# Kernel optimization log

Measured on AMD Instinct MI355X. Metric: run time of the kernel, lower is better.

## Reference

```python
import jax, jax.numpy as jnp
import numpy as np

B, C, V = 65536, 2, 3          # batch of coords, coord_dim, value_dim
D, K, S = 64, 1024, 4          # latent_dim, num_codes, num_latent_vectors (VQ stages)
H, L, F = 1024, 5, 25          # hidden_size, num_layers, num_freqs
IN = C * (2 * F + 1)           # 102: positional-encoded decoder input
COMMIT = 0.25


def setup_inputs() -> dict:
    key = jax.random.key(0)
    ks = jax.random.split(key, 12)
    coords = jax.random.uniform(ks[0], (B, C), jnp.float32, -1.0, 1.0)
    latents = jax.random.normal(ks[1], (1, S, D), jnp.float32)
    cb = jax.random.normal(ks[2], (S, K, D), jnp.float32)
    codebooks = cb / jnp.linalg.norm(cb, axis=-1, keepdims=True)  # unit-norm init as in module
    mod_W = jax.random.normal(ks[3], (L, D, H), jnp.float32) / np.sqrt(D)
    mod_b = jax.random.normal(ks[4], (L, H), jnp.float32) * 0.01
    dec_W0 = jax.random.normal(ks[5], (IN, H), jnp.float32) / np.sqrt(IN)
    dec_b0 = jax.random.normal(ks[6], (H,), jnp.float32) * 0.01
    dec_Wh = jax.random.normal(ks[7], (L - 1, H, H), jnp.float32) / np.sqrt(H)
    dec_bh = jax.random.normal(ks[8], (L - 1, H), jnp.float32) * 0.01
    dec_Wout = jax.random.normal(ks[9], (H, V), jnp.float32) / np.sqrt(H)
    dec_bout = jax.random.normal(ks[10], (V,), jnp.float32) * 0.01
    return dict(coords=coords, latent_idx=0, latents=latents, codebooks=codebooks,
                mod_W=mod_W, mod_b=mod_b, dec_W0=dec_W0, dec_b0=dec_b0,
                dec_Wh=dec_Wh, dec_bh=dec_bh, dec_Wout=dec_Wout, dec_bout=dec_bout)


def _vq(z, emb):
    # z: (1, D), emb: (K, D) -> squared-distance argmin + straight-through
    d = jnp.sum(z * z, axis=1, keepdims=True) - 2.0 * (z @ emb.T) + jnp.sum(emb * emb, axis=1)
    idx = jnp.argmin(d, axis=1)               # (1,)
    z_q = emb[idx]                            # (1, D)
    z_q_st = z_q + jax.lax.stop_gradient(z - z_q)   # fwd value == z, grad flows to embedding
    loss = COMMIT * jnp.mean((jax.lax.stop_gradient(z_q) - z) ** 2)
    return z_q_st, idx, loss


def reference(coords, latent_idx, latents, codebooks, mod_W, mod_b,
              dec_W0, dec_b0, dec_Wh, dec_bh, dec_Wout, dec_bout):
    img = latents[latent_idx]                 # (S, D)
    z_q_sum = jnp.zeros((1, D), coords.dtype)
    residual_target = jnp.zeros((1, D), coords.dtype)
    total_vq_loss = 0.0
    idxs = []
    for s in range(S):                        # residual VQ over fixed small #stages
        z_stage = img[s:s + 1]
        if s == 0:
            residual_target = z_stage
            z_cur = z_stage
        else:
            residual_target = residual_target + z_stage
            z_cur = residual_target - jax.lax.stop_gradient(z_q_sum)
        z_q_st, idx, l = _vq(z_cur, codebooks[s])
        z_q_sum = z_q_sum + z_q_st
        total_vq_loss = total_vq_loss + l
        idxs.append(idx)
    # modulation betas from the (same-for-all-rows) quantized latent; broadcast over B
    betas = jnp.einsum('od,ldh->loh', z_q_sum, mod_W) + mod_b[:, None, :]   # (L, 1, H)
    # positional encoding: [x, sin(pi*f0*x), cos(pi*f0*x), sin(pi*f1*x), ...]
    freqs = 2.0 ** jnp.arange(F, dtype=coords.dtype)
    ang = coords[:, None, :] * (freqs[None, :, None] * jnp.pi)              # (B, F, C)
    pe = jnp.concatenate(
        [coords, jnp.stack([jnp.sin(ang), jnp.cos(ang)], axis=2).reshape(coords.shape[0], -1)],
        axis=-1)                                                            # (B, IN)
    h = jax.nn.relu(pe @ dec_W0 + dec_b0 + betas[0])
    for i in range(L - 1):
        h = jax.nn.relu(h @ dec_Wh[i] + dec_bh[i] + betas[i + 1])
    values = h @ dec_Wout + dec_bout                                        # (B, V)
    return values, jnp.stack(idxs), total_vq_loss
```

## Files before the change

kernel.cpp:

```cpp
#include <hip/hip_runtime.h>
#include <hip/hip_bf16.h>
#include <stdint.h>

#define NB   65536
#define NC   2
#define NV   3
#define ND   64
#define NK   1024
#define NS   4
#define NH   1024
#define NL   5
#define NF   25
#define NIN  102
#define K0P  128

typedef float f32x4  __attribute__((ext_vector_type(4)));
typedef float f32x16 __attribute__((ext_vector_type(16)));
typedef int   i32x4  __attribute__((ext_vector_type(4)));
typedef int   i32x8  __attribute__((ext_vector_type(8)));
typedef unsigned char u8;

__device__ __forceinline__ void load_lds16(const void* g, void* l) {
    __builtin_amdgcn_global_load_lds(
        (const __attribute__((address_space(1))) void*)g,
        (__attribute__((address_space(3))) void*)l,
        16, 0, 0);
}

__device__ __forceinline__ u8 to_fp8(float x) {
    return (u8)(__builtin_amdgcn_cvt_pk_fp8_f32(x, 0.0f, 0, false) & 0xff);
}

__device__ __forceinline__ f32x16 mfma32(i32x8 wf, i32x8 af, f32x16 c) {
    return __builtin_amdgcn_mfma_scale_f32_32x32x64_f8f6f4(
        wf, af, c, 0, 0,
        0, 0x79797979,
        0, 0x7f7f7f7f);
}


__global__ __launch_bounds__(1024) void vq_kernel(
    const float* __restrict__ latents, const int* __restrict__ latent_idx,
    const float* __restrict__ codebooks, float* __restrict__ zq_out,
    float* __restrict__ out) {
    __shared__ float zcur[ND], resid[ND], zqsum[ND], ssq[ND];
    __shared__ float sDw[16];
    __shared__ int   sKw[16];
    __shared__ int   sBest;
    int t = threadIdx.x, lane = t & 63, wv = t >> 6;
    const float* img = latents + (size_t)latent_idx[0] * (NS * ND);
    if (t < ND) { resid[t] = 0.f; zqsum[t] = 0.f; }
    __syncthreads();
    float lossAcc = 0.f;
    for (int s = 0; s < NS; s++) {
        if (t < ND) {
            float iv = img[s * ND + t];
            float r  = resid[t] + iv;
            resid[t] = r;
            zcur[t]  = (s == 0) ? iv : (r - zqsum[t]);
        }
        __syncthreads();
        float zz = 0.f;
#pragma unroll
        for (int d = 0; d < ND; d++) { float z = zcur[d]; zz += z * z; }
        const float4* e4 = (const float4*)(codebooks + ((size_t)s * NK + t) * ND);
        float dot = 0.f, ee = 0.f;
#pragma unroll
        for (int i = 0; i < 16; i++) {
            float4 v = e4[i];
            dot += zcur[4 * i + 0] * v.x; dot += zcur[4 * i + 1] * v.y;
            dot += zcur[4 * i + 2] * v.z; dot += zcur[4 * i + 3] * v.w;
            ee  += v.x * v.x; ee += v.y * v.y; ee += v.z * v.z; ee += v.w * v.w;
        }
        float dmin = zz - 2.0f * dot + ee;
        int   kmin = t;
#pragma unroll
        for (int m = 1; m < 64; m <<= 1) {
            float d2 = __shfl_xor(dmin, m);
            int   k2 = __shfl_xor(kmin, m);
            if (d2 < dmin || (d2 == dmin && k2 < kmin)) { dmin = d2; kmin = k2; }
        }
        if (lane == 0) { sDw[wv] = dmin; sKw[wv] = kmin; }
        __syncthreads();
        if (t == 0) {
            float bd = sDw[0]; int bk = sKw[0];
            for (int w = 1; w < 16; w++) {
                float d2 = sDw[w]; int k2 = sKw[w];
                if (d2 < bd || (d2 == bd && k2 < bk)) { bd = d2; bk = k2; }
            }
            sBest = bk;
            out[NB * NV + s] = (float)bk;
        }
        __syncthreads();
        int best = sBest;
        const float* eb = codebooks + ((size_t)s * NK + best) * ND;
        if (t < ND) {
            float zq = eb[t];
            float d  = zq - zcur[t];
            ssq[t]   = d * d;
            zqsum[t] = zqsum[t] + (zq + (zcur[t] - zq));
        }
        __syncthreads();
        if (t == 0) {
            float sum = 0.f;
            for (int d = 0; d < ND; d++) sum += ssq[d];
            lossAcc += 0.25f * (sum / (float)ND);
        }
    }
    if (t < ND) zq_out[t] = zqsum[t];
    if (t == 0) out[NB * NV + NS] = lossAcc;
}

__global__ __launch_bounds__(256) void betas_kernel(
    const float* __restrict__ zq, const float* __restrict__ mod_W,
    const float* __restrict__ mod_b, const float* __restrict__ b0,
    const float* __restrict__ bh, float* __restrict__ bb) {
    int g = blockIdx.x * 256 + threadIdx.x;
    int l = g >> 10, n = g & 1023;
    float acc = mod_b[g];
    for (int d = 0; d < ND; d++) acc += zq[d] * mod_W[(size_t)(l * ND + d) * NH + n];
    acc += (l == 0) ? b0[n] : bh[(size_t)(l - 1) * NH + n];
    bb[g] = acc;
}

__global__ __launch_bounds__(256) void init_out_kernel(
    const float* __restrict__ bout, float* __restrict__ out) {
    int g = blockIdx.x * 256 + threadIdx.x;
    out[g] = bout[g % NV];
}

__global__ __launch_bounds__(256) void prep_kernel(
    const float* __restrict__ src, u8* __restrict__ dst, int Ks, int Kp) {
    __shared__ float tile[32][33];
    src += (size_t)blockIdx.z * Ks * NH;
    dst += (size_t)blockIdx.z * NH * Kp;
    int k0 = blockIdx.x * 32, n0 = blockIdx.y * 32;
    int tx = threadIdx.x, ty = threadIdx.y;
    for (int i = 0; i < 4; i++) {
        int k = k0 + ty + i * 8;
        int n = n0 + tx;
        tile[ty + i * 8][tx] = (k < Ks) ? src[(size_t)k * NH + n] : 0.0f;
    }
    __syncthreads();
    for (int i = 0; i < 4; i++) {
        int n = n0 + ty + i * 8;
        int k = k0 + tx;
        int bn = n >> 7, j32 = (n >> 5) & 3, r32 = n & 31;
        int ks = k >> 6, kh = (k >> 5) & 1, h = (k >> 4) & 1, b16 = k & 15;
        size_t flat = (size_t)bn * ((size_t)Kp * 128)
                    + ((size_t)(((ks * 4 + j32) * 2 + h) * 2 + kh) * 32 + r32) * 16 + b16;
        dst[flat] = to_fp8(tile[tx][ty + i * 8] * 64.0f);
    }
}

__device__ __forceinline__ float pe_val(const float* coords, int m, int k) {
    if (k < 2) return coords[m * 2 + k];
    if (k >= NIN) return 0.0f;
    int u = k - 2;
    int f = u >> 2, r = u & 3;
    float c = coords[m * 2 + (r & 1)];
    float a = c * __builtin_ldexpf(3.14159274101257324f, f);
    return (r < 2) ? sinf(a) : cosf(a);
}

__global__ __launch_bounds__(256) void pe_kernel(
    const float* __restrict__ coords, u8* __restrict__ pe) {
    int g = blockIdx.x * 256 + threadIdx.x;
    int m = g >> 5, k4 = (g & 31) * 4;
    float v0 = pe_val(coords, m, k4 + 0);
    float v1 = pe_val(coords, m, k4 + 1);
    float v2 = pe_val(coords, m, k4 + 2);
    float v3 = pe_val(coords, m, k4 + 3);
    int p = __builtin_amdgcn_cvt_pk_fp8_f32(v0, v1, 0, false);
    p     = __builtin_amdgcn_cvt_pk_fp8_f32(v2, v3, p, true);
    int m32 = m >> 5, r32 = m & 31;
    int ks = k4 >> 6, kh = (k4 >> 5) & 1, h = (k4 >> 4) & 1, b16 = k4 & 15;
    *(int*)(pe + (size_t)(m32 * 2 + ks) * 2048
            + ((h * 2 + kh) * 32 + r32) * 16 + b16) = p;
}

template <int MODE, int KT>
__global__ __launch_bounds__(256, 2) void gemm_kernel(
    const u8* __restrict__ A, const u8* __restrict__ W,
    const float* __restrict__ bb, u8* __restrict__ O,
    const float* __restrict__ Wout, float* __restrict__ out, int Mb) {
    __shared__ __align__(16) u8 smem[32768];
    int t   = threadIdx.x;
    int fid = blockIdx.x;
    int xcd = fid & 7;
    int j8  = fid >> 3;
    int bn  = j8 & 7;
    int bm  = xcd * (Mb >> 3) + (j8 >> 3);
    int lane = t & 63, wm = t >> 6;
    int r32  = lane & 31, hl = lane >> 5;
    constexpr int nIt = KT >> 7;
    constexpr int nKs = KT >> 6;

    const u8* wslab = W + (size_t)bn * ((size_t)KT * 128);
    const u8* abase = A + ((size_t)(bm * 8 + wm * 2) * nKs) * 2048 + lane * 16;

    f32x16 acc[2][4];
#pragma unroll
    for (int i = 0; i < 2; i++)
#pragma unroll
        for (int j = 0; j < 4; j++)
#pragma unroll
            for (int e = 0; e < 16; e++) acc[i][j][e] = 0.0f;

#define LOAD_AF(dst, KS)                                                       \
    {                                                                          \
        _Pragma("unroll")                                                      \
        for (int mt = 0; mt < 2; mt++) {                                       \
            const u8* p = abase + ((size_t)mt * nKs + (KS)) * 2048;            \
            i32x4 lo = *(const i32x4*)(p);                                     \
            i32x4 hi = *(const i32x4*)(p + 1024);                              \
            dst[mt] = __builtin_shufflevector(lo, hi, 0, 1, 2, 3, 4, 5, 6, 7); \
        }                                                                      \
    }
#define MFMA_HALF(base, KSL, AF)                                               \
    {                                                                          \
        _Pragma("unroll")                                                      \
        for (int j = 0; j < 4; j++) {                                          \
            const u8* c = (base) + (KSL) * 8192 + j * 2048 + lane * 16;        \
            i32x4 lo = *(const i32x4*)(c);                                     \
            i32x4 hi = *(const i32x4*)(c + 1024);                              \
            i32x8 wf = __builtin_shufflevector(lo, hi, 0, 1, 2, 3, 4, 5, 6, 7);\
            acc[0][j] = mfma32(wf, AF[0], acc[0][j]);                          \
            acc[1][j] = mfma32(wf, AF[1], acc[1][j]);                          \
        }                                                                      \
    }

    if constexpr (nIt == 1) {
#pragma unroll
        for (int p = 0; p < 4; p++) {
            int g = p * 256 + t;
            load_lds16((const void*)(wslab + g * 16), (void*)(smem + g * 16));
        }
        i32x8 af0[2], af1[2];
        LOAD_AF(af0, 0)
        LOAD_AF(af1, 1)
        __syncthreads();
        MFMA_HALF(smem, 0, af0)
        MFMA_HALF(smem, 1, af1)
        __syncthreads();
    } else {
#pragma unroll
        for (int p = 0; p < 4; p++) {
            int g = p * 256 + t;
            load_lds16((const void*)(wslab + g * 16), (void*)(smem + g * 16));
        }
        i32x8 afc0[2], afc1[2], afn0[2], afn1[2];
        LOAD_AF(afc0, 0)
        LOAD_AF(afc1, 1)
        __syncthreads();

#pragma unroll 1
        for (int it = 0; it < nIt; it++) {
            u8* bufc = smem + ((it & 1) ? 16384 : 0);
            u8* bufn = smem + ((it & 1) ? 0 : 16384);
            if (it + 1 < nIt) {
                const u8* ws = wslab + (size_t)(it + 1) * 16384;
#pragma unroll
                for (int p = 0; p < 4; p++) {
                    int g = p * 256 + t;
                    load_lds16((const void*)(ws + g * 16), (void*)(bufn + g * 16));
                }
                LOAD_AF(afn0, 2 * (it + 1))
                LOAD_AF(afn1, 2 * (it + 1) + 1)
            }
            MFMA_HALF(bufc, 0, afc0)
            MFMA_HALF(bufc, 1, afc1)
            __syncthreads();
#pragma unroll
            for (int mt = 0; mt < 2; mt++) { afc0[mt] = afn0[mt]; afc1[mt] = afn1[mt]; }
        }
    }
#undef LOAD_AF
#undef MFMA_HALF

    if constexpr (MODE == 0) {
        u8* eb = smem;
#pragma unroll
        for (int mt = 0; mt < 2; mt++) {
#pragma unroll
            for (int nt = 0; nt < 4; nt++) {
                int kh  = nt & 1;
                int seg = (wm * 2 + mt) * 2 + (nt >> 1);
#pragma unroll
                for (int g = 0; g < 4; g++) {
                    int nbase = nt * 32 + 8 * g + 4 * hl;
                    f32x4 b4 = *(const f32x4*)(bb + bn * 128 + nbase);
                    float v0 = fmaxf(acc[mt][nt][4 * g + 0] + b4[0], 0.0f);
                    float v1 = fmaxf(acc[mt][nt][4 * g + 1] + b4[1], 0.0f);
                    float v2 = fmaxf(acc[mt][nt][4 * g + 2] + b4[2], 0.0f);
                    float v3 = fmaxf(acc[mt][nt][4 * g + 3] + b4[3], 0.0f);
                    int p = __builtin_amdgcn_cvt_pk_fp8_f32(v0, v1, 0, false);
                    p     = __builtin_amdgcn_cvt_pk_fp8_f32(v2, v3, p, true);
                    int h   = g >> 1;
                    int idx = seg * 2048 + ((h * 2 + kh) * 32 + r32) * 16
                            + ((8 * g + 4 * hl) & 15);
                    *(int*)(eb + idx) = p;
                }
            }
        }
        __syncthreads();
#pragma unroll
        for (int rd = 0; rd < 8; rd++) {
            int g2  = rd * 256 + t;
            int seg = g2 >> 7, off = (g2 & 127) * 16;
            int m32l = seg >> 1, ksl = seg & 1;
            i32x4 v = *(const i32x4*)(eb + seg * 2048 + off);
            *(i32x4*)(O + ((size_t)((bm * 8 + m32l) * (NH >> 6) + bn * 2 + ksl)) * 2048
                      + off) = v;
        }
    } else {
#pragma unroll
        for (int mt = 0; mt < 2; mt++) {
            float p0 = 0.f, p1 = 0.f, p2 = 0.f;
#pragma unroll
            for (int nt = 0; nt < 4; nt++) {
#pragma unroll
                for (int g = 0; g < 4; g++) {
                    int nbase = bn * 128 + nt * 32 + 8 * g + 4 * hl;
                    f32x4 b4 = *(const f32x4*)(bb + nbase);
#pragma unroll
                    for (int rr = 0; rr < 4; rr++) {
                        float val = fmaxf(acc[mt][nt][4 * g + rr] + b4[rr], 0.0f);
                        const float* wo = Wout + (size_t)(nbase + rr) * NV;
                        p0 += val * wo[0]; p1 += val * wo[1]; p2 += val * wo[2];
                    }
                }
            }
            p0 += __shfl_xor(p0, 32);
            p1 += __shfl_xor(p1, 32);
            p2 += __shfl_xor(p2, 32);
            if (hl == 0) {
                int m = bm * 256 + wm * 64 + mt * 32 + r32;
                atomicAdd(&out[(size_t)m * NV + 0], p0);
                atomicAdd(&out[(size_t)m * NV + 1], p1);
                atomicAdd(&out[(size_t)m * NV + 2], p2);
            }
        }
    }
}

extern "C" void kernel_launch(void* const* d_in, const int* in_sizes, int n_in,
                              void* d_out, int out_size, void* d_ws, size_t ws_size,
                              hipStream_t stream) {
    const float* coords     = (const float*)d_in[0];
    const int*   latent_idx = (const int*)d_in[1];
    const float* latents    = (const float*)d_in[2];
    const float* codebooks  = (const float*)d_in[3];
    const float* mod_W      = (const float*)d_in[4];
    const float* mod_b      = (const float*)d_in[5];
    const float* dec_W0     = (const float*)d_in[6];
    const float* dec_b0     = (const float*)d_in[7];
    const float* dec_Wh     = (const float*)d_in[8];
    const float* dec_bh     = (const float*)d_in[9];
    const float* dec_Wout   = (const float*)d_in[10];
    const float* dec_bout   = (const float*)d_in[11];
    float* out = (float*)d_out;

    char* wsb = (char*)d_ws;
    float* zq  = (float*)(wsb + 0);
    float* bb  = (float*)(wsb + 256);
    u8*    W0T = (u8*)(wsb + 20736);
    u8*    WhT = (u8*)(wsb + 151808);
    const size_t fixed_end = 4346368;

    int Bc = 65536;
    while (Bc > 2048 && fixed_end + 2 * (size_t)Bc * NH > ws_size)
        Bc >>= 1;
    int Mb = Bc / 256;

    u8* hA = (u8*)(wsb + fixed_end);
    u8* hB = hA + (size_t)Bc * NH;
    u8* pe = hB;

    vq_kernel<<<1, 1024, 0, stream>>>(latents, latent_idx, codebooks, zq, out);
    betas_kernel<<<20, 256, 0, stream>>>(zq, mod_W, mod_b, dec_b0, dec_bh, bb);
    init_out_kernel<<<(NB * NV) / 256, 256, 0, stream>>>(dec_bout, out);
    prep_kernel<<<dim3(4, 32, 1), dim3(32, 8), 0, stream>>>(dec_W0, W0T, NIN, K0P);
    prep_kernel<<<dim3(32, 32, 4), dim3(32, 8), 0, stream>>>(dec_Wh, WhT, NH, NH);

    for (int c0 = 0; c0 < NB; c0 += Bc) {
        pe_kernel<<<(Bc * 32) / 256, 256, 0, stream>>>(coords + (size_t)c0 * NC, pe);
        gemm_kernel<0, K0P><<<8 * Mb, 256, 0, stream>>>(
            pe, W0T, bb + 0 * NH, hA, nullptr, nullptr, Mb);
        gemm_kernel<0, NH><<<8 * Mb, 256, 0, stream>>>(
            hA, WhT + 0 * (size_t)NH * NH, bb + 1 * NH, hB, nullptr, nullptr, Mb);
        gemm_kernel<0, NH><<<8 * Mb, 256, 0, stream>>>(
            hB, WhT + 1 * (size_t)NH * NH, bb + 2 * NH, hA, nullptr, nullptr, Mb);
        gemm_kernel<0, NH><<<8 * Mb, 256, 0, stream>>>(
            hA, WhT + 2 * (size_t)NH * NH, bb + 3 * NH, hB, nullptr, nullptr, Mb);
        gemm_kernel<1, NH><<<8 * Mb, 256, 0, stream>>>(
            hB, WhT + 3 * (size_t)NH * NH, bb + 4 * NH, nullptr,
            dec_Wout, out + (size_t)c0 * NV, Mb);
    }
}
```

Measured before the change: 466.6 us.

## Fuse positional encoding into first GEMM and merge small setup kernels

Computes the positional-encoding fragments directly in registers inside the first-layer GEMM from coords, which removes the separate pe_kernel and its FP8 write/read round trip. Merges the betas and output-init kernels into one launch, and merges the two weight-prep launches into one grid. Replaces the serial loss sum in the VQ kernel with a wavefront shuffle reduction and adds a compiler memory barrier in the GEMM prefetch. The trade-off is that each first-layer block now recomputes sin/cos, once per one of the 8 column blocks that share a row tile.

```diff
diff --git a/kernel.cpp b/kernel.cpp
--- a/kernel.cpp
+++ b/kernel.cpp
@@ -101,39 +101,48 @@
             zqsum[t] = zqsum[t] + (zq + (zcur[t] - zq));
         }
         __syncthreads();
-        if (t == 0) {
-            float sum = 0.f;
-            for (int d = 0; d < ND; d++) sum += ssq[d];
-            lossAcc += 0.25f * (sum / (float)ND);
+        if (t < 64) {
+            float sum = ssq[t];
+#pragma unroll
+            for (int m = 1; m < 64; m <<= 1) sum += __shfl_xor(sum, m);
+            if (t == 0) lossAcc += 0.25f * (sum / (float)ND);
         }
     }
     if (t < ND) zq_out[t] = zqsum[t];
     if (t == 0) out[NB * NV + NS] = lossAcc;
 }
 
-__global__ __launch_bounds__(256) void betas_kernel(
+__global__ __launch_bounds__(256) void betas_init_kernel(
     const float* __restrict__ zq, const float* __restrict__ mod_W,
     const float* __restrict__ mod_b, const float* __restrict__ b0,
-    const float* __restrict__ bh, float* __restrict__ bb) {
-    int g = blockIdx.x * 256 + threadIdx.x;
-    int l = g >> 10, n = g & 1023;
-    float acc = mod_b[g];
-    for (int d = 0; d < ND; d++) acc += zq[d] * mod_W[(size_t)(l * ND + d) * NH + n];
-    acc += (l == 0) ? b0[n] : bh[(size_t)(l - 1) * NH + n];
-    bb[g] = acc;
-}
-
-__global__ __launch_bounds__(256) void init_out_kernel(
+    const float* __restrict__ bh, float* __restrict__ bb,
     const float* __restrict__ bout, float* __restrict__ out) {
     int g = blockIdx.x * 256 + threadIdx.x;
-    out[g] = bout[g % NV];
+    if (g < 5120) {
+        int l = g >> 10, n = g & 1023;
+        float acc = mod_b[g];
+        for (int d = 0; d < ND; d++) acc += zq[d] * mod_W[(size_t)(l * ND + d) * NH + n];
+        acc += (l == 0) ? b0[n] : bh[(size_t)(l - 1) * NH + n];
+        bb[g] = acc;
+    } else {
+        int o = g - 5120;
+        if (o < NB * NV) out[o] = bout[o % NV];
+    }
 }
 
 __global__ __launch_bounds__(256) void prep_kernel(
-    const float* __restrict__ src, u8* __restrict__ dst, int Ks, int Kp) {
+    const float* __restrict__ dec_W0, const float* __restrict__ dec_Wh,
+    u8* __restrict__ W0T, u8* __restrict__ WhT) {
+    int z = blockIdx.z;
+    const float* src; u8* dst; int Ks, Kp;
+    if (z < 4) {
+        src = dec_Wh + (size_t)z * NH * NH; dst = WhT + (size_t)z * NH * NH;
+        Ks = NH; Kp = NH;
+    } else {
+        if (blockIdx.x >= 4) return;
+        src = dec_W0; dst = W0T; Ks = NIN; Kp = K0P;
+    }
     __shared__ float tile[32][33];
-    src += (size_t)blockIdx.z * Ks * NH;
-    dst += (size_t)blockIdx.z * NH * Kp;
     int k0 = blockIdx.x * 32, n0 = blockIdx.y * 32;
     int tx = threadIdx.x, ty = threadIdx.y;
     for (int i = 0; i < 4; i++) {
@@ -153,37 +162,22 @@
     }
 }
 
-__device__ __forceinline__ float pe_val(const float* coords, int m, int k) {
-    if (k < 2) return coords[m * 2 + k];
+__device__ __forceinline__ float pe_val2(float cx, float cy, int k) {
+    if (k < 2) return (k == 0) ? cx : cy;
     if (k >= NIN) return 0.0f;
     int u = k - 2;
     int f = u >> 2, r = u & 3;
-    float c = coords[m * 2 + (r & 1)];
+    float c = (r & 1) ? cy : cx;
     float a = c * __builtin_ldexpf(3.14159274101257324f, f);
     return (r < 2) ? sinf(a) : cosf(a);
-}
-
-__global__ __launch_bounds__(256) void pe_kernel(
-    const float* __restrict__ coords, u8* __restrict__ pe) {
-    int g = blockIdx.x * 256 + threadIdx.x;
-    int m = g >> 5, k4 = (g & 31) * 4;
-    float v0 = pe_val(coords, m, k4 + 0);
-    float v1 = pe_val(coords, m, k4 + 1);
-    float v2 = pe_val(coords, m, k4 + 2);
-    float v3 = pe_val(coords, m, k4 + 3);
-    int p = __builtin_amdgcn_cvt_pk_fp8_f32(v0, v1, 0, false);
-    p     = __builtin_amdgcn_cvt_pk_fp8_f32(v2, v3, p, true);
-    int m32 = m >> 5, r32 = m & 31;
-    int ks = k4 >> 6, kh = (k4 >> 5) & 1, h = (k4 >> 4) & 1, b16 = k4 & 15;
-    *(int*)(pe + (size_t)(m32 * 2 + ks) * 2048
-            + ((h * 2 + kh) * 32 + r32) * 16 + b16) = p;
 }
 
 template <int MODE, int KT>
 __global__ __launch_bounds__(256, 2) void gemm_kernel(
     const u8* __restrict__ A, const u8* __restrict__ W,
     const float* __restrict__ bb, u8* __restrict__ O,
-    const float* __restrict__ Wout, float* __restrict__ out, int Mb) {
+    const float* __restrict__ Wout, float* __restrict__ out,
+    const float* __restrict__ coords, int Mb) {
     __shared__ __align__(16) u8 smem[32768];
     int t   = threadIdx.x;
     int fid = blockIdx.x;
@@ -237,8 +231,25 @@
             load_lds16((const void*)(wslab + g * 16), (void*)(smem + g * 16));
         }
         i32x8 af0[2], af1[2];
-        LOAD_AF(af0, 0)
-        LOAD_AF(af1, 1)
+#pragma unroll
+        for (int mt = 0; mt < 2; mt++) {
+            int m = bm * 256 + wm * 64 + mt * 32 + r32;
+            float cx = coords[m * 2 + 0], cy = coords[m * 2 + 1];
+#pragma unroll
+            for (int ks = 0; ks < 2; ks++) {
+                i32x8 v;
+#pragma unroll
+                for (int e = 0; e < 8; e++) {
+                    int kb = ks * 64 + hl * 32 + e * 4;
+                    int p = __builtin_amdgcn_cvt_pk_fp8_f32(
+                        pe_val2(cx, cy, kb + 0), pe_val2(cx, cy, kb + 1), 0, false);
+                    p = __builtin_amdgcn_cvt_pk_fp8_f32(
+                        pe_val2(cx, cy, kb + 2), pe_val2(cx, cy, kb + 3), p, true);
+                    v[e] = p;
+                }
+                if (ks == 0) af0[mt] = v; else af1[mt] = v;
+            }
+        }
         __syncthreads();
         MFMA_HALF(smem, 0, af0)
         MFMA_HALF(smem, 1, af1)
@@ -267,6 +278,7 @@
                 }
                 LOAD_AF(afn0, 2 * (it + 1))
                 LOAD_AF(afn1, 2 * (it + 1) + 1)
+                asm volatile("" ::: "memory");
             }
             MFMA_HALF(bufc, 0, afc0)
             MFMA_HALF(bufc, 1, afc1)
@@ -375,26 +387,28 @@
 
     u8* hA = (u8*)(wsb + fixed_end);
     u8* hB = hA + (size_t)Bc * NH;
-    u8* pe = hB;
 
     vq_kernel<<<1, 1024, 0, stream>>>(latents, latent_idx, codebooks, zq, out);
-    betas_kernel<<<20, 256, 0, stream>>>(zq, mod_W, mod_b, dec_b0, dec_bh, bb);
-    init_out_kernel<<<(NB * NV) / 256, 256, 0, stream>>>(dec_bout, out);
-    prep_kernel<<<dim3(4, 32, 1), dim3(32, 8), 0, stream>>>(dec_W0, W0T, NIN, K0P);
-    prep_kernel<<<dim3(32, 32, 4), dim3(32, 8), 0, stream>>>(dec_Wh, WhT, NH, NH);
+    betas_init_kernel<<<(5120 + NB * NV) / 256, 256, 0, stream>>>(
+        zq, mod_W, mod_b, dec_b0, dec_bh, bb, dec_bout, out);
+    prep_kernel<<<dim3(32, 32, 5), dim3(32, 8), 0, stream>>>(
+        dec_W0, dec_Wh, W0T, WhT);
 
     for (int c0 = 0; c0 < NB; c0 += Bc) {
-        pe_kernel<<<(Bc * 32) / 256, 256, 0, stream>>>(coords + (size_t)c0 * NC, pe);
         gemm_kernel<0, K0P><<<8 * Mb, 256, 0, stream>>>(
-            pe, W0T, bb + 0 * NH, hA, nullptr, nullptr, Mb);
+            nullptr, W0T, bb + 0 * NH, hA, nullptr, nullptr,
+            coords + (size_t)c0 * NC, Mb);
         gemm_kernel<0, NH><<<8 * Mb, 256, 0, stream>>>(
-            hA, WhT + 0 * (size_t)NH * NH, bb + 1 * NH, hB, nullptr, nullptr, Mb);
+            hA, WhT + 0 * (size_t)NH * NH, bb + 1 * NH, hB, nullptr, nullptr,
+            nullptr, Mb);
         gemm_kernel<0, NH><<<8 * Mb, 256, 0, stream>>>(
-            hB, WhT + 1 * (size_t)NH * NH, bb + 2 * NH, hA, nullptr, nullptr, Mb);
+            hB, WhT + 1 * (size_t)NH * NH, bb + 2 * NH, hA, nullptr, nullptr,
+            nullptr, Mb);
         gemm_kernel<0, NH><<<8 * Mb, 256, 0, stream>>>(
-            hA, WhT + 2 * (size_t)NH * NH, bb + 3 * NH, hB, nullptr, nullptr, Mb);
+            hA, WhT + 2 * (size_t)NH * NH, bb + 3 * NH, hB, nullptr, nullptr,
+            nullptr, Mb);
         gemm_kernel<1, NH><<<8 * Mb, 256, 0, stream>>>(
             hB, WhT + 3 * (size_t)NH * NH, bb + 4 * NH, nullptr,
-            dec_Wout, out + (size_t)c0 * NV, Mb);
-    }
-}
+            dec_Wout, out + (size_t)c0 * NV, nullptr, Mb);
+    }
+}
```

New measurement: 554.8 us. 1.19x slower.
